# Optimization experiments

Measured on AMD Instinct MI355X. Metric: run time of the kernel, lower is better.

## Reference

```python
import jax, jax.numpy as jnp
import numpy as np

N = 50000   # nodes
E = 800000  # edges (avg degree 16)
D = 128     # input feature dim
H = 128     # hidden dim
C = 10      # num classes
G = 16      # graphs in batch


def setup_inputs() -> dict:
    key = jax.random.key(0)
    ks = jax.random.split(key, 12)
    def w(k, shape):
        return jax.random.normal(k, shape, jnp.float32) / np.sqrt(shape[0]).astype(np.float32)
    return {
        "h": jax.random.normal(ks[0], (N, D), jnp.float32),
        "src": jax.random.randint(ks[1], (E,), 0, N, jnp.int32),
        "dst": jax.random.randint(ks[2], (E,), 0, N, jnp.int32),
        "graph_ids": jnp.sort(jax.random.randint(ks[3], (N,), 0, G, jnp.int32)),
        "W1a": w(ks[4], (D, H)), "b1a": jnp.zeros((H,), jnp.float32),
        "W2a": w(ks[5], (H, H)), "b2a": jnp.zeros((H,), jnp.float32),
        "W1b": w(ks[6], (H, H)), "b1b": jnp.zeros((H,), jnp.float32),
        "W2b": w(ks[7], (H, H)), "b2b": jnp.zeros((H,), jnp.float32),
        "Wc1": w(ks[8], (H, H)), "bc1": jnp.zeros((H,), jnp.float32),
        "Wc2": w(ks[9], (H, C)), "bc2": jnp.zeros((C,), jnp.float32),
    }


def _gin_layer(h, src, dst, W1, b1, W2, b2):
    # GIN aggregation, eps=0: z_i = h_i + sum_{j in N(i)} h_j
    agg = jax.ops.segment_sum(h[src], dst, num_segments=N)
    z = h + agg
    # 2-layer MLP apply function with relu activation ('relu' arg of GINLayer)
    z = jax.nn.relu(z @ W1 + b1)
    return jax.nn.relu(z @ W2 + b2)


def reference(h, src, dst, graph_ids, W1a, b1a, W2a, b2a,
              W1b, b1b, W2b, b2b, Wc1, bc1, Wc2, bc2):
    h = _gin_layer(h, src, dst, W1a, b1a, W2a, b2a)   # [N, H]
    h = _gin_layer(h, src, dst, W1b, b1b, W2b, b2b)   # [N, H]
    # dgl.mean_nodes over the batched graph
    sums = jax.ops.segment_sum(h, graph_ids, num_segments=G)                # [G, H]
    cnts = jax.ops.segment_sum(jnp.ones((N, 1), h.dtype), graph_ids, num_segments=G)
    h_g = sums / jnp.maximum(cnts, 1.0)
    # cls MLP: linear -> relu -> linear (logits)
    out = jax.nn.relu(h_g @ Wc1 + bc1) @ Wc2 + bc2    # [G, C]
    return out
```

## Files before the change

kernel.cpp:

```cpp
#include <hip/hip_runtime.h>
#include <stdint.h>

#define NN 50000
#define EE 800000
#define DD 128
#define GG 16
#define CC 10
#define NBK 196
#define BCH 4096
#define SMAX 5120
#define FT (NBK * NBK)
#define NSCN ((FT + 255) / 256)
#define NT 782

typedef unsigned short u16;
typedef __bf16 bf16x8 __attribute__((ext_vector_type(8)));
typedef float f32x4 __attribute__((ext_vector_type(4)));
typedef unsigned int u32x4 __attribute__((ext_vector_type(4)));
typedef float fl4 __attribute__((ext_vector_type(4)));

__device__ inline u16 f2bf(float f) {
    unsigned u = __float_as_uint(f);
    u = u + 0x7fffu + ((u >> 16) & 1u);
    return (u16)(u >> 16);
}
__device__ inline unsigned pack2(float a, float b) {
    return (unsigned)f2bf(a) | ((unsigned)f2bf(b) << 16);
}
__device__ inline float bf2f(unsigned bits16) { return __uint_as_float(bits16 << 16); }
__device__ inline void acc8(float* a, uint4 v) {
    a[0] += __uint_as_float(v.x << 16); a[1] += __uint_as_float(v.x & 0xffff0000u);
    a[2] += __uint_as_float(v.y << 16); a[3] += __uint_as_float(v.y & 0xffff0000u);
    a[4] += __uint_as_float(v.z << 16); a[5] += __uint_as_float(v.z & 0xffff0000u);
    a[6] += __uint_as_float(v.w << 16); a[7] += __uint_as_float(v.w & 0xffff0000u);
}
__device__ inline void mand(uint4& v, int p) {
    unsigned m = p ? 0xffffffffu : 0u;
    v.x &= m; v.y &= m; v.z &= m; v.w &= m;
}
__device__ inline void nt_store16(void* p, uint4 v) {
    u32x4 x; x.x = v.x; x.y = v.y; x.z = v.z; x.w = v.w;
    __builtin_nontemporal_store(x, (u32x4*)p);
}
__device__ inline float4 nt_loadf4(const float* p) {
    fl4 x = __builtin_nontemporal_load((const fl4*)p);
    float4 r; r.x = x.x; r.y = x.y; r.z = x.z; r.w = x.w;
    return r;
}

#define PZ (GG * DD + 16)
#define PC (NN * DD / 4)
#define PW (4 * DD * DD)
#define PTOT (PZ + PC + PW)
#define PBLK ((PTOT + 255) / 256)

__global__ __launch_bounds__(256) void prepsort_kernel(
    const float* __restrict__ h,
    const float* __restrict__ a, const float* __restrict__ b,
    const float* __restrict__ c, const float* __restrict__ d,
    int* __restrict__ zbase, u16* __restrict__ H0, u16* __restrict__ wt,
    const int* __restrict__ dst, int* __restrict__ counts) {
    __shared__ int hist[NBK];
    int blk = blockIdx.x, t = threadIdx.x;
    if (blk < NBK) {
        for (int i = t; i < NBK; i += 256) hist[i] = 0;
        __syncthreads();
        int e0 = blk * BCH, e1 = min(e0 + BCH, EE);
        for (int e = e0 + t; e < e1; e += 256) atomicAdd(&hist[dst[e] >> 8], 1);
        __syncthreads();
        for (int i = t; i < NBK; i += 256) counts[i * NBK + blk] = hist[i];
        return;
    }
    int i = (blk - NBK) * 256 + t;
    if (i < PZ) { zbase[i] = 0; return; }
    i -= PZ;
    if (i < PC) {
        int j = i * 4;
        float4 v = nt_loadf4(h + j);
        ushort4 o;
        o.x = f2bf(v.x); o.y = f2bf(v.y); o.z = f2bf(v.z); o.w = f2bf(v.w);
        *(ushort4*)(H0 + j) = o;
        return;
    }
    i -= PC;
    if (i < PW) {
        int m = i >> 14, r = i & 16383, k = r >> 7, j = r & 127;
        const float* W = (m == 0) ? a : (m == 1) ? b : (m == 2) ? c : d;
        wt[(m << 14) + (j << 7) + k] = f2bf(W[(k << 7) + j]);
    }
}

__global__ __launch_bounds__(256) void scanAB_kernel(int* __restrict__ counts,
                                                     int* __restrict__ bsum,
                                                     int* __restrict__ done,
                                                     const int* __restrict__ gids,
                                                     int* __restrict__ gstart) {
    __shared__ int tmp[256];
    __shared__ int amLast;
    int t = threadIdx.x, idx = blockIdx.x * 256 + t;
    int v = (idx < FT) ? counts[idx] : 0;
    tmp[t] = v; __syncthreads();
    for (int off = 1; off < 256; off <<= 1) {
        int x = (t >= off) ? tmp[t - off] : 0;
        __syncthreads();
        tmp[t] += x;
        __syncthreads();
    }
    if (idx < FT) counts[idx] = tmp[t] - v;
    if (t == 255) atomicExch(&bsum[blockIdx.x], tmp[255]);
    __threadfence();
    __syncthreads();
    if (t == 0) amLast = (atomicAdd(&done[0], 1) == NSCN - 1);
    __syncthreads();
    if (!amLast) return;
    if (t <= GG) {
        int lo = 0, hi = NN;
        while (lo < hi) { int mid = (lo + hi) >> 1; if (gids[mid] < t) lo = mid + 1; else hi = mid; }
        gstart[t] = lo;
    }
    int bv = (t < NSCN) ? atomicAdd(&bsum[t], 0) : 0;
    tmp[t] = bv; __syncthreads();
    for (int off = 1; off < 256; off <<= 1) {
        int x = (t >= off) ? tmp[t - off] : 0;
        __syncthreads();
        tmp[t] += x;
        __syncthreads();
    }
    if (t < NSCN) bsum[t] = tmp[t] - bv;
}

__global__ __launch_bounds__(256) void sortP3_kernel(const int* __restrict__ src,
                                                     const int* __restrict__ dst,
                                                     const int* __restrict__ counts,
                                                     const int* __restrict__ bsum,
                                                     int* __restrict__ epack) {
    __shared__ int lhist[NBK + 1];
    __shared__ int lcur[NBK];
    __shared__ int goff[NBK];
    __shared__ int tmp[256];
    __shared__ int sbuf[BCH];
    int b = blockIdx.x, t = threadIdx.x;
    int e0 = b * BCH, e1 = min(e0 + BCH, EE), n = e1 - e0;

    for (int i = t; i < NBK; i += 256) lhist[i] = 0;
    __syncthreads();
    for (int e = e0 + t; e < e1; e += 256) atomicAdd(&lhist[dst[e] >> 8], 1);
    __syncthreads();
    int v = (t < NBK) ? lhist[t] : 0;
    tmp[t] = v; __syncthreads();
    for (int off = 1; off < 256; off <<= 1) {
        int x = (t >= off) ? tmp[t - off] : 0;
        __syncthreads();
        tmp[t] += x;
        __syncthreads();
    }
    if (t < NBK) {
        int excl = tmp[t] - v;
        lcur[t] = excl;
        lhist[t] = excl;
        int fi = t * NBK + b;
        goff[t] = counts[fi] + bsum[fi >> 8] - excl;
    }
    if (t == 0) lhist[NBK] = n;
    __syncthreads();
    for (int e = e0 + t; e < e1; e += 256) {
        int dd = dst[e], s = src[e];
        int p = atomicAdd(&lcur[dd >> 8], 1);
        sbuf[p] = (s << 8) | (dd & 255);
    }
    __syncthreads();
    for (int i = t; i < n; i += 256) {
        int pk = sbuf[i];
        int lo = 0, hi = NBK - 1;
        while (lo < hi) { int mid = (lo + hi + 1) >> 1; if (lhist[mid] <= i) lo = mid; else hi = mid - 1; }
        epack[goff[lo] + i] = pk;
    }
}

__global__ __launch_bounds__(256) void sortP4_kernel(const int* __restrict__ epack,
                                                     const int* __restrict__ counts,
                                                     const int* __restrict__ bsum,
                                                     int* __restrict__ offs,
                                                     int* __restrict__ ssrc) {
    __shared__ int hist[256];
    __shared__ int curs[256];
    __shared__ int stage[SMAX];
    int j = blockIdx.x, t = threadIdx.x;
    int n0 = j << 8;
    int fi0 = j * NBK;
    int b0 = counts[fi0] + bsum[fi0 >> 8];
    int b1;
    if (j < NBK - 1) { int fi1 = (j + 1) * NBK; b1 = counts[fi1] + bsum[fi1 >> 8]; }
    else b1 = EE;
    hist[t] = 0;
    __syncthreads();
    for (int e = b0 + t; e < b1; e += 256) atomicAdd(&hist[epack[e] & 255], 1);
    __syncthreads();
    int deg = hist[t];
    for (int off = 1; off < 256; off <<= 1) {
        int x = (t >= off) ? hist[t - off] : 0;
        __syncthreads();
        hist[t] += x;
        __syncthreads();
    }
    int loff = hist[t] - deg;
    curs[t] = loff;
    if (n0 + t <= NN) offs[n0 + t] = b0 + loff;
    __syncthreads();
    for (int e = b0 + t; e < b1; e += 256) {
        int pk = epack[e];
        int p = atomicAdd(&curs[pk & 255], 1);
        stage[p] = pk >> 8;
    }
    __syncthreads();
    int n = b1 - b0;
    for (int i = t; i < n; i += 256) ssrc[b0 + i] = stage[i];
}

__global__ __launch_bounds__(256) void agg_kernel(
    const u16* __restrict__ Hin, const int* __restrict__ offs,
    const int* __restrict__ ssrc, u16* __restrict__ Z) {
    int node = blockIdx.x * 16 + (threadIdx.x >> 4);
    int lid = threadIdx.x & 15;
    if (node >= NN) return;
    int foff = lid * 8;
    const u16* base = Hin + foff;

    float acc[8] = {0.f, 0.f, 0.f, 0.f, 0.f, 0.f, 0.f, 0.f};
    uint4 vs = *(const uint4*)(base + (size_t)node * DD);
    int e0 = offs[node], e1 = offs[node + 1];
    acc8(acc, vs);

    int nch = (e1 - e0 + 7) >> 3;
    if (nch > 0) {
        int elast = e1 - 1;
        int i0 = ssrc[e0];
        int i1 = ssrc[min(e0 + 1, elast)];
        int i2 = ssrc[min(e0 + 2, elast)];
        int i3 = ssrc[min(e0 + 3, elast)];
        int i4 = ssrc[min(e0 + 4, elast)];
        int i5 = ssrc[min(e0 + 5, elast)];
        int i6 = ssrc[min(e0 + 6, elast)];
        int i7 = ssrc[min(e0 + 7, elast)];
        int eb = e0;
        for (int c = 0; c < nch; c++) {
            int ebn = eb + 8;
            int n0 = i0, n1 = i1, n2 = i2, n3 = i3, n4 = i4, n5 = i5, n6 = i6, n7 = i7;
            if (c + 1 < nch) {
                n0 = ssrc[ebn];
                n1 = ssrc[min(ebn + 1, elast)];
                n2 = ssrc[min(ebn + 2, elast)];
                n3 = ssrc[min(ebn + 3, elast)];
                n4 = ssrc[min(ebn + 4, elast)];
                n5 = ssrc[min(ebn + 5, elast)];
                n6 = ssrc[min(ebn + 6, elast)];
                n7 = ssrc[min(ebn + 7, elast)];
            }
            uint4 v0 = *(const uint4*)(base + (size_t)i0 * DD);
            uint4 v1 = *(const uint4*)(base + (size_t)i1 * DD);
            uint4 v2 = *(const uint4*)(base + (size_t)i2 * DD);
            uint4 v3 = *(const uint4*)(base + (size_t)i3 * DD);
            uint4 v4 = *(const uint4*)(base + (size_t)i4 * DD);
            uint4 v5 = *(const uint4*)(base + (size_t)i5 * DD);
            uint4 v6 = *(const uint4*)(base + (size_t)i6 * DD);
            uint4 v7 = *(const uint4*)(base + (size_t)i7 * DD);
            mand(v1, eb + 1 < e1); mand(v2, eb + 2 < e1); mand(v3, eb + 3 < e1);
            mand(v4, eb + 4 < e1); mand(v5, eb + 5 < e1); mand(v6, eb + 6 < e1);
            mand(v7, eb + 7 < e1);
            acc8(acc, v0); acc8(acc, v1); acc8(acc, v2); acc8(acc, v3);
            acc8(acc, v4); acc8(acc, v5); acc8(acc, v6); acc8(acc, v7);
            i0 = n0; i1 = n1; i2 = n2; i3 = n3; i4 = n4; i5 = n5; i6 = n6; i7 = n7;
            eb = ebn;
        }
    }
    uint4 o;
    o.x = pack2(acc[0], acc[1]); o.y = pack2(acc[2], acc[3]);
    o.z = pack2(acc[4], acc[5]); o.w = pack2(acc[6], acc[7]);
    nt_store16(Z + (size_t)node * DD + foff, o);
}

__global__ __launch_bounds__(256, 1) void mlp_kernel(
    const u16* __restrict__ Zin, const u16* __restrict__ Wt1, const float* __restrict__ b1,
    const u16* __restrict__ Wt2, const float* __restrict__ b2,
    u16* __restrict__ Hout, const int* __restrict__ gids, float* __restrict__ pool,
    int* __restrict__ done2, const int* __restrict__ gstart,
    const float* __restrict__ Wc1, const float* __restrict__ bc1,
    const float* __restrict__ Wc2, const float* __restrict__ bc2,
    float* __restrict__ out) {
    __shared__ __align__(16) u16 w1f[16384];
    __shared__ __align__(16) u16 yb[64][136];
    __shared__ int amLast;
    const int tid = threadIdx.x;
    const int wave = tid >> 6;
    const int lane = tid & 63;
    const int m16 = lane & 15;
    const int quad = lane >> 4;

    for (int cidx = tid; cidx < 2048; cidx += 256) {
        int ln = cidx & 63, nt = (cidx >> 6) & 7, kk = cidx >> 9;
        int gofs = ((nt * 16 + (ln & 15)) << 7) + kk * 32 + (ln >> 4) * 8;
        *(uint4*)&w1f[cidx * 8] = *(const uint4*)(Wt1 + gofs);
    }
    bf16x8 w2r[4][8];
#pragma unroll
    for (int kk = 0; kk < 4; kk++)
#pragma unroll
        for (int nt = 0; nt < 8; nt++)
            w2r[kk][nt] = *(const bf16x8*)(Wt2 + ((nt * 16 + m16) << 7) + kk * 32 + quad * 8);
    float bias1[8], bias2[8];
#pragma unroll
    for (int nt = 0; nt < 8; nt++) {
        bias1[nt] = b1[nt * 16 + m16];
        bias2[nt] = b2[nt * 16 + m16];
    }
    __syncthreads();

    int tile = blockIdx.x;
    bf16x8 afr[4], afrN[4];
    {
        size_t row = (size_t)(tile * 64 + wave * 16 + m16);
#pragma unroll
        for (int kk = 0; kk < 4; kk++)
            afr[kk] = *(const bf16x8*)(Zin + row * DD + kk * 32 + quad * 8);
    }
    for (; tile < NT; tile += 256) {
        int nxt = tile + 256;
        if (nxt < NT) {
            size_t row = (size_t)(nxt * 64 + wave * 16 + m16);
#pragma unroll
            for (int kk = 0; kk < 4; kk++)
                afrN[kk] = *(const bf16x8*)(Zin + row * DD + kk * 32 + quad * 8);
        }
        const int row0 = tile * 64 + wave * 16;

        f32x4 acc[8];
#pragma unroll
        for (int nt = 0; nt < 8; nt++) acc[nt] = (f32x4){0.f, 0.f, 0.f, 0.f};
#pragma unroll
        for (int kk = 0; kk < 4; kk++) {
#pragma unroll
            for (int nt = 0; nt < 8; nt++) {
                bf16x8 bfr = *(const bf16x8*)&w1f[(((kk * 8 + nt) * 64) + lane) * 8];
                acc[nt] = __builtin_amdgcn_mfma_f32_16x16x32_bf16(afr[kk], bfr, acc[nt], 0, 0, 0);
            }
        }
#pragma unroll
        for (int nt = 0; nt < 8; nt++) {
            int col = nt * 16 + m16;
#pragma unroll
            for (int r = 0; r < 4; r++) {
                float yv = acc[nt][r] + bias1[nt];
                yv = yv > 0.f ? yv : 0.f;
                yb[wave * 16 + quad * 4 + r][col] = f2bf(yv);
            }
        }

        bf16x8 afr2[4];
#pragma unroll
        for (int kk = 0; kk < 4; kk++)
            afr2[kk] = *(const bf16x8*)&yb[wave * 16 + m16][kk * 32 + quad * 8];
#pragma unroll
        for (int nt = 0; nt < 8; nt++) acc[nt] = (f32x4){0.f, 0.f, 0.f, 0.f};
#pragma unroll
        for (int kk = 0; kk < 4; kk++) {
#pragma unroll
            for (int nt = 0; nt < 8; nt++)
                acc[nt] = __builtin_amdgcn_mfma_f32_16x16x32_bf16(afr2[kk], w2r[kk][nt], acc[nt], 0, 0, 0);
        }
#pragma unroll
        for (int nt = 0; nt < 8; nt++) {
            int col = nt * 16 + m16;
#pragma unroll
            for (int r = 0; r < 4; r++) {
                float ov = acc[nt][r] + bias2[nt];
                ov = ov > 0.f ? ov : 0.f;
                yb[wave * 16 + quad * 4 + r][col] = f2bf(ov);
            }
        }
        if (!pool) {
#pragma unroll
            for (int p = 0; p < 4; p++) {
                int idx = p * 64 + lane;
                int r = idx >> 4, ch = idx & 15;
                int grow = row0 + r;
                if (grow < NN)
                    *(uint4*)(Hout + (size_t)grow * DD + ch * 8) = *(const uint4*)&yb[wave * 16 + r][ch * 8];
            }
        } else {
            int prow = row0 + m16;
            int g = gids[min(prow, NN - 1)];
#pragma unroll
            for (int fsel = 0; fsel < 2; fsel++) {
                int f = lane + fsel * 64;
                float s = 0.f;
                int cur = __shfl(g, 0);
                for (int r = 0; r < 16; r++) {
                    int gr = __shfl(g, r);
                    float v = (row0 + r < NN) ? bf2f((unsigned)yb[wave * 16 + r][f]) : 0.f;
                    if (gr != cur) { atomicAdd(&pool[cur * DD + f], s); s = 0.f; cur = gr; }
                    s += v;
                }
                atomicAdd(&pool[cur * DD + f], s);
            }
        }
#pragma unroll
        for (int kk = 0; kk < 4; kk++) afr[kk] = afrN[kk];
    }

    if (pool) {
        __threadfence();
        if (tid == 0) amLast = (atomicAdd(done2, 1) == 255);
        __syncthreads();
        if (amLast) {
            __shared__ float hg[2][128];
            __shared__ float y1[2][128];
            int half = tid >> 7, f = tid & 127;
            for (int gp = 0; gp < GG; gp += 2) {
                int g = gp + half;
                int cnt = gstart[g + 1] - gstart[g];
                float inv = 1.f / (float)(cnt > 1 ? cnt : 1);
                hg[half][f] = atomicAdd(&pool[g * DD + f], 0.f) * inv;
                __syncthreads();
                float a2 = bc1[f];
                for (int k = 0; k < DD; k++) a2 += hg[half][k] * Wc1[k * DD + f];
                y1[half][f] = a2 > 0.f ? a2 : 0.f;
                __syncthreads();
                if (f < CC) {
                    float o = bc2[f];
                    for (int k = 0; k < DD; k++) o += y1[half][k] * Wc2[k * CC + f];
                    out[g * CC + f] = o;
                }
                __syncthreads();
            }
        }
    }
}

extern "C" void kernel_launch(void* const* d_in, const int* in_sizes, int n_in,
                              void* d_out, int out_size, void* d_ws, size_t ws_size,
                              hipStream_t stream) {
    const float* h    = (const float*)d_in[0];
    const int*   src  = (const int*)d_in[1];
    const int*   dst  = (const int*)d_in[2];
    const int*   gids = (const int*)d_in[3];
    const float* W1a  = (const float*)d_in[4];
    const float* b1a  = (const float*)d_in[5];
    const float* W2a  = (const float*)d_in[6];
    const float* b2a  = (const float*)d_in[7];
    const float* W1b  = (const float*)d_in[8];
    const float* b1b  = (const float*)d_in[9];
    const float* W2b  = (const float*)d_in[10];
    const float* b2b  = (const float*)d_in[11];
    const float* Wc1  = (const float*)d_in[12];
    const float* bc1  = (const float*)d_in[13];
    const float* Wc2  = (const float*)d_in[14];
    const float* bc2  = (const float*)d_in[15];
    float* out = (float*)d_out;

    char* ws = (char*)d_ws;
    u16*   H0     = (u16*)(ws);
    u16*   H1     = (u16*)(ws + 12800000);
    u16*   H2     = (u16*)(ws + 25600000);
    u16*   Wt     = (u16*)(ws + 38400000);
    float* pool   = (float*)(ws + 38531072);
    int*   done   = (int*)(ws + 38539264);
    int*   offs   = (int*)(ws + 38539328);
    int*   ssrc   = (int*)(ws + 38739332);
    int*   gstart = (int*)(ws + 41939332);
    int*   counts = (int*)(ws + 41939400);
    int*   bsum   = (int*)(ws + 42093064);
    int*   epack  = (int*)(ws + 42093696);
    u16*   Z1     = H2;
    u16*   Z2     = H0;

    prepsort_kernel<<<dim3(NBK + PBLK), dim3(256), 0, stream>>>(
        h, W1a, W2a, W1b, W2b, (int*)pool, H0, Wt, dst, counts);
    scanAB_kernel<<<dim3(NSCN), dim3(256), 0, stream>>>(counts, bsum, done, gids, gstart);
    sortP3_kernel<<<dim3(NBK), dim3(256), 0, stream>>>(src, dst, counts, bsum, epack);
    sortP4_kernel<<<dim3(NBK), dim3(256), 0, stream>>>(epack, counts, bsum, offs, ssrc);
    agg_kernel<<<dim3((NN + 15) / 16), dim3(256), 0, stream>>>(H0, offs, ssrc, Z1);
    mlp_kernel<<<dim3(256), dim3(256), 0, stream>>>(Z1, Wt, b1a, Wt + 16384, b2a, H1,
                                                    gids, nullptr, done + 1, gstart,
                                                    Wc1, bc1, Wc2, bc2, out);
    agg_kernel<<<dim3((NN + 15) / 16), dim3(256), 0, stream>>>(H1, offs, ssrc, Z2);
    mlp_kernel<<<dim3(256), dim3(256), 0, stream>>>(Z2, Wt + 32768, b1b, Wt + 49152, b2b, H2,
                                                    gids, pool, done + 1, gstart,
                                                    Wc1, bc1, Wc2, bc2, out);
}
```

Before: 294.4 us.

## Stage second MLP weights in LDS and split classifier into separate kernel

The second-layer weight fragments now live in shared memory and are read from LDS inside the MFMA loop, instead of being held as 32 bf16x8 vectors in registers. This frees a large block of VGPRs in the MLP kernel at the cost of extra LDS reads per tile. The last-block detection with atomic counter, threadfence and serial classifier tail is removed and replaced by a small 16-block cls_kernel launched afterwards. That swaps an in-kernel tail for one extra launch.

```diff
diff --git a/kernel.cpp b/kernel.cpp
--- a/kernel.cpp
+++ b/kernel.cpp
@@ -282,31 +282,24 @@
 __global__ __launch_bounds__(256, 1) void mlp_kernel(
     const u16* __restrict__ Zin, const u16* __restrict__ Wt1, const float* __restrict__ b1,
     const u16* __restrict__ Wt2, const float* __restrict__ b2,
-    u16* __restrict__ Hout, const int* __restrict__ gids, float* __restrict__ pool,
-    int* __restrict__ done2, const int* __restrict__ gstart,
-    const float* __restrict__ Wc1, const float* __restrict__ bc1,
-    const float* __restrict__ Wc2, const float* __restrict__ bc2,
-    float* __restrict__ out) {
+    u16* __restrict__ Hout, const int* __restrict__ gids, float* __restrict__ pool) {
     __shared__ __align__(16) u16 w1f[16384];
+    __shared__ __align__(16) u16 w2f[16384];
     __shared__ __align__(16) u16 yb[64][136];
-    __shared__ int amLast;
     const int tid = threadIdx.x;
     const int wave = tid >> 6;
     const int lane = tid & 63;
     const int m16 = lane & 15;
     const int quad = lane >> 4;
 
-    for (int cidx = tid; cidx < 2048; cidx += 256) {
-        int ln = cidx & 63, nt = (cidx >> 6) & 7, kk = cidx >> 9;
+    for (int cidx = tid; cidx < 4096; cidx += 256) {
+        int c = cidx & 2047;
+        int ln = c & 63, nt = (c >> 6) & 7, kk = c >> 9;
         int gofs = ((nt * 16 + (ln & 15)) << 7) + kk * 32 + (ln >> 4) * 8;
-        *(uint4*)&w1f[cidx * 8] = *(const uint4*)(Wt1 + gofs);
-    }
-    bf16x8 w2r[4][8];
-#pragma unroll
-    for (int kk = 0; kk < 4; kk++)
-#pragma unroll
-        for (int nt = 0; nt < 8; nt++)
-            w2r[kk][nt] = *(const bf16x8*)(Wt2 + ((nt * 16 + m16) << 7) + kk * 32 + quad * 8);
+        u16* dstb = (cidx < 2048) ? w1f : w2f;
+        const u16* srcb = (cidx < 2048) ? Wt1 : Wt2;
+        *(uint4*)&dstb[c * 8] = *(const uint4*)(srcb + gofs);
+    }
     float bias1[8], bias2[8];
 #pragma unroll
     for (int nt = 0; nt < 8; nt++) {
@@ -364,8 +357,10 @@
 #pragma unroll
         for (int kk = 0; kk < 4; kk++) {
 #pragma unroll
-            for (int nt = 0; nt < 8; nt++)
-                acc[nt] = __builtin_amdgcn_mfma_f32_16x16x32_bf16(afr2[kk], w2r[kk][nt], acc[nt], 0, 0, 0);
+            for (int nt = 0; nt < 8; nt++) {
+                bf16x8 bfr = *(const bf16x8*)&w2f[(((kk * 8 + nt) * 64) + lane) * 8];
+                acc[nt] = __builtin_amdgcn_mfma_f32_16x16x32_bf16(afr2[kk], bfr, acc[nt], 0, 0, 0);
+            }
         }
 #pragma unroll
         for (int nt = 0; nt < 8; nt++) {
@@ -406,33 +401,28 @@
 #pragma unroll
         for (int kk = 0; kk < 4; kk++) afr[kk] = afrN[kk];
     }
-
-    if (pool) {
-        __threadfence();
-        if (tid == 0) amLast = (atomicAdd(done2, 1) == 255);
-        __syncthreads();
-        if (amLast) {
-            __shared__ float hg[2][128];
-            __shared__ float y1[2][128];
-            int half = tid >> 7, f = tid & 127;
-            for (int gp = 0; gp < GG; gp += 2) {
-                int g = gp + half;
-                int cnt = gstart[g + 1] - gstart[g];
-                float inv = 1.f / (float)(cnt > 1 ? cnt : 1);
-                hg[half][f] = atomicAdd(&pool[g * DD + f], 0.f) * inv;
-                __syncthreads();
-                float a2 = bc1[f];
-                for (int k = 0; k < DD; k++) a2 += hg[half][k] * Wc1[k * DD + f];
-                y1[half][f] = a2 > 0.f ? a2 : 0.f;
-                __syncthreads();
-                if (f < CC) {
-                    float o = bc2[f];
-                    for (int k = 0; k < DD; k++) o += y1[half][k] * Wc2[k * CC + f];
-                    out[g * CC + f] = o;
-                }
-                __syncthreads();
-            }
-        }
+}
+
+__global__ void cls_kernel(const float* __restrict__ pool, const int* __restrict__ gstart,
+                           const float* __restrict__ Wc1, const float* __restrict__ bc1,
+                           const float* __restrict__ Wc2, const float* __restrict__ bc2,
+                           float* __restrict__ out) {
+    __shared__ float hg[128];
+    __shared__ float y1[128];
+    int g = blockIdx.x;
+    int t = threadIdx.x;
+    int cnt = gstart[g + 1] - gstart[g];
+    float inv = 1.f / (float)(cnt > 1 ? cnt : 1);
+    hg[t] = pool[g * DD + t] * inv;
+    __syncthreads();
+    float a = bc1[t];
+    for (int k = 0; k < DD; k++) a += hg[k] * Wc1[k * DD + t];
+    y1[t] = a > 0.f ? a : 0.f;
+    __syncthreads();
+    if (t < CC) {
+        float o = bc2[t];
+        for (int k = 0; k < DD; k++) o += y1[k] * Wc2[k * CC + t];
+        out[g * CC + t] = o;
     }
 }
 
@@ -479,11 +469,8 @@
     sortP3_kernel<<<dim3(NBK), dim3(256), 0, stream>>>(src, dst, counts, bsum, epack);
     sortP4_kernel<<<dim3(NBK), dim3(256), 0, stream>>>(epack, counts, bsum, offs, ssrc);
     agg_kernel<<<dim3((NN + 15) / 16), dim3(256), 0, stream>>>(H0, offs, ssrc, Z1);
-    mlp_kernel<<<dim3(256), dim3(256), 0, stream>>>(Z1, Wt, b1a, Wt + 16384, b2a, H1,
-                                                    gids, nullptr, done + 1, gstart,
-                                                    Wc1, bc1, Wc2, bc2, out);
+    mlp_kernel<<<dim3(256), dim3(256), 0, stream>>>(Z1, Wt, b1a, Wt + 16384, b2a, H1, gids, nullptr);
     agg_kernel<<<dim3((NN + 15) / 16), dim3(256), 0, stream>>>(H1, offs, ssrc, Z2);
-    mlp_kernel<<<dim3(256), dim3(256), 0, stream>>>(Z2, Wt + 32768, b1b, Wt + 49152, b2b, H2,
-                                                    gids, pool, done + 1, gstart,
-                                                    Wc1, bc1, Wc2, bc2, out);
-}
+    mlp_kernel<<<dim3(256), dim3(256), 0, stream>>>(Z2, Wt + 32768, b1b, Wt + 49152, b2b, H2, gids, pool);
+    cls_kernel<<<dim3(GG), dim3(128), 0, stream>>>(pool, gstart, Wc1, bc1, Wc2, bc2, out);
+}
```

Measured after the change: 263.5 us. 1.12x faster.
